# Performance work log

Hardware: AMD Instinct MI355X
Metric: run time of the kernel (lower is better)

The kernel has to match this reference:

```python
import jax, jax.numpy as jnp
import numpy as np

N = 100000   # nodes
E = 1600000  # edges (before self-loops)
D = 128      # in_feats
H = 128      # n_hidden


def setup_inputs() -> dict:
    key = jax.random.key(0)
    k = jax.random.split(key, 6)
    x = jax.random.normal(k[0], (N, D), dtype=jnp.float32)
    src = jax.random.randint(k[1], (E,), 0, N, dtype=jnp.int32)
    dst = jax.random.randint(k[2], (E,), 0, N, dtype=jnp.int32)
    W1 = jax.random.normal(k[3], (D, H), dtype=jnp.float32) / np.float32(np.sqrt(D))
    b1 = jnp.zeros((H,), jnp.float32)
    W2 = jax.random.normal(k[4], (H, H), dtype=jnp.float32) / np.float32(np.sqrt(H))
    b2 = jnp.zeros((H,), jnp.float32)
    return {"x": x, "src": src, "dst": dst, "W1": W1, "b1": b1, "W2": W2, "b2": b2}


def _gcn(x, src, dst, W1, b1, W2, b2):
    n = x.shape[0]
    # add_self_loop(g)
    loops = jnp.arange(n, dtype=src.dtype)
    s = jnp.concatenate([src, loops])
    d = jnp.concatenate([dst, loops])
    ones = jnp.ones((s.shape[0],), dtype=x.dtype)
    deg_out = jax.ops.segment_sum(ones, s, num_segments=n)  # src out-degree
    deg_in = jax.ops.segment_sum(ones, d, num_segments=n)   # dst in-degree
    # DGL GraphConv norm='both': D_out^{-1/2} on source side, D_in^{-1/2} on dest side
    norm_out = jax.lax.rsqrt(jnp.maximum(deg_out, 1.0))[:, None]
    norm_in = jax.lax.rsqrt(jnp.maximum(deg_in, 1.0))[:, None]

    def layer(h, W, b):
        h = h * norm_out                                   # [n, f]
        agg = jax.ops.segment_sum(h[s], d, num_segments=n)  # gather + scatter-add over edges
        return (agg * norm_in) @ W + b

    h = layer(x, W1, b1)
    # dropout p=0 -> identity
    h = layer(h, W2, b2)
    return h


def reference(x, src, dst, W1, b1, W2, b2):
    return _gcn(x, src, dst, W1, b1, W2, b2)
```

## Files before the change

kernel.cpp:

```cpp
#include <hip/hip_runtime.h>

#define FD 128
#define SHIFT 10
#define BNODES 1024
#define NBK 128
#define CHUNK 4096
#define ST 512
#define NE 12

typedef unsigned int u32;
typedef unsigned short u16;
typedef unsigned char u8;
typedef __attribute__((ext_vector_type(8))) short short8;
typedef __attribute__((ext_vector_type(4))) float f32x4;
typedef __attribute__((ext_vector_type(4))) u32 u32x4;

__device__ inline u16 f2bf(float f) {
  u32 u = __float_as_uint(f);
  u += 0x7fffu + ((u >> 16) & 1u);
  return (u16)(u >> 16);
}
__device__ inline float bf2f(u16 h) { return __uint_as_float((u32)h << 16); }

__global__ __launch_bounds__(512) void k_hist(const int* __restrict__ src,
                                              const int* __restrict__ dst,
                                              int* __restrict__ bcntD,
                                              int* __restrict__ bcntS,
                                              int e, int n, int nbuck) {
  __shared__ int shD[NBK];
  __shared__ int shS[NBK];
  int tid = threadIdx.x;
  if (tid < NBK) { shD[tid] = 0; shS[tid] = 0; }
  __syncthreads();
  int total = e + n;
  for (int t = blockIdx.x * blockDim.x + tid; t < total; t += gridDim.x * blockDim.x) {
    if (t < e) {
      atomicAdd(&shD[dst[t] >> SHIFT], 1);
      atomicAdd(&shS[src[t] >> SHIFT], 1);
    } else {
      atomicAdd(&shD[(t - e) >> SHIFT], 1);
    }
  }
  __syncthreads();
  if (tid < nbuck) {
    if (shD[tid]) atomicAdd(&bcntD[tid], shD[tid]);
    if (shS[tid]) atomicAdd(&bcntS[tid], shS[tid]);
  }
}

__global__ __launch_bounds__(NBK) void k_bscan(
    const int* __restrict__ bcntD, const int* __restrict__ bcntS,
    int* __restrict__ bbaseD, int* __restrict__ bcurD,
    int* __restrict__ bbaseS, int* __restrict__ bcurS,
    int nbuck, int totalD, int totalS) {
  __shared__ int shD[NBK];
  __shared__ int shS[NBK];
  int tid = threadIdx.x;
  int vD = (tid < nbuck) ? bcntD[tid] : 0;
  int vS = (tid < nbuck) ? bcntS[tid] : 0;
  shD[tid] = vD; shS[tid] = vS;
  __syncthreads();
  for (int off = 1; off < NBK; off <<= 1) {
    int aD = (tid >= off) ? shD[tid - off] : 0;
    int aS = (tid >= off) ? shS[tid - off] : 0;
    __syncthreads();
    shD[tid] += aD; shS[tid] += aS;
    __syncthreads();
  }
  if (tid < nbuck) {
    int exD = shD[tid] - vD; bbaseD[tid] = exD; bcurD[tid] = exD;
    int exS = shS[tid] - vS; bbaseS[tid] = exS; bcurS[tid] = exS;
  }
  if (tid == 0) { bbaseD[nbuck] = totalD; bbaseS[nbuck] = totalS; }
}

__global__ __launch_bounds__(ST) void k_scatter(
    const int* __restrict__ src, const int* __restrict__ dst,
    int* __restrict__ bcurD, int* __restrict__ bcurS,
    u32* __restrict__ pairs, u16* __restrict__ pairs2,
    int e, int n, int nbuck) {
  __shared__ int histD[NBK], exclD[NBK], gbaseD[NBK], rankD[NBK];
  __shared__ int histS[NBK], exclS[NBK], gbaseS[NBK], rankS[NBK];
  __shared__ u32 stgv[CHUNK];
  __shared__ u8  stgb[CHUNK];
  __shared__ u16 stg2[CHUNK];
  __shared__ u8  stg2b[CHUNK];
  int tid = threadIdx.x;
  int c0 = blockIdx.x * CHUNK;
  int total = e + n;
  if (tid < NBK) { histD[tid] = 0; histS[tid] = 0; }
  __syncthreads();
  u32 pv_[8]; int bD_[8], bS_[8]; bool v_[8], vs_[8];
  #pragma unroll
  for (int i = 0; i < 8; ++i) {
    int t = c0 + i * ST + tid;
    v_[i] = (t < total);
    vs_[i] = (t < e);
    pv_[i] = 0; bD_[i] = 0; bS_[i] = 0;
    if (v_[i]) {
      int s, d;
      if (vs_[i]) { s = src[t]; d = dst[t]; }
      else        { s = t - e;  d = s; }
      pv_[i] = ((u32)(d & (BNODES - 1)) << 22) | (u32)s;
      bD_[i] = d >> SHIFT;
      atomicAdd(&histD[bD_[i]], 1);
      if (vs_[i]) { bS_[i] = s >> SHIFT; atomicAdd(&histS[bS_[i]], 1); }
    }
  }
  __syncthreads();
  int hD = 0, hS = 0;
  if (tid < NBK) { hD = histD[tid]; hS = histS[tid]; }
  __syncthreads();
  for (int off = 1; off < NBK; off <<= 1) {
    int aD = 0, aS = 0;
    if (tid < NBK && tid >= off) { aD = histD[tid - off]; aS = histS[tid - off]; }
    __syncthreads();
    if (tid < NBK) { histD[tid] += aD; histS[tid] += aS; }
    __syncthreads();
  }
  if (tid < NBK) {
    int exD = histD[tid] - hD; exclD[tid] = exD; rankD[tid] = exD;
    int exS = histS[tid] - hS; exclS[tid] = exS; rankS[tid] = exS;
    gbaseD[tid] = (tid < nbuck && hD > 0) ? atomicAdd(&bcurD[tid], hD) : 0;
    gbaseS[tid] = (tid < nbuck && hS > 0) ? atomicAdd(&bcurS[tid], hS) : 0;
  }
  __syncthreads();
  #pragma unroll
  for (int i = 0; i < 8; ++i) {
    if (v_[i]) {
      int p = atomicAdd(&rankD[bD_[i]], 1);
      stgv[p] = pv_[i];
      stgb[p] = (u8)bD_[i];
    }
    if (vs_[i]) {
      int p = atomicAdd(&rankS[bS_[i]], 1);
      stg2[p] = (u16)(pv_[i] & (BNODES - 1));
      stg2b[p] = (u8)bS_[i];
    }
  }
  __syncthreads();
  int V = min(CHUNK, total - c0);
  for (int j = tid; j < V; j += ST) {
    int b = stgb[j];
    pairs[gbaseD[b] + (j - exclD[b])] = stgv[j];
  }
  int V2 = min(CHUNK, e - c0);
  for (int j = tid; j < V2; j += ST) {
    int b = stg2b[j];
    pairs2[gbaseS[b] + (j - exclS[b])] = stg2[j];
  }
}

__global__ __launch_bounds__(1024) void k_build(
    const u32* __restrict__ pairs, const int* __restrict__ bbase,
    const u16* __restrict__ pairs2, const int* __restrict__ bbaseS,
    int* __restrict__ rp, int* __restrict__ col,
    float* __restrict__ nin, float* __restrict__ nout,
    int n, int nbuck, int total) {
  __shared__ int cnt[BNODES];
  __shared__ int off_[BNODES];
  __shared__ int cur[BNODES];
  int tid = threadIdx.x;
  if (blockIdx.x >= (unsigned)nbuck) {
    int b = blockIdx.x - nbuck;
    int base = bbaseS[b], end = bbaseS[b + 1];
    cnt[tid] = 0;
    __syncthreads();
    for (int t = base + tid; t < end; t += 1024)
      atomicAdd(&cnt[(int)pairs2[t]], 1);
    __syncthreads();
    int node = (b << SHIFT) + tid;
    if (node < n) nout[node] = rsqrtf((float)(cnt[tid] + 1));
    return;
  }
  int b = blockIdx.x;
  int base = bbase[b], end = bbase[b + 1];
  int node0 = b << SHIFT;
  cnt[tid] = 0;
  __syncthreads();
  for (int t = base + tid; t < end; t += 1024)
    atomicAdd(&cnt[(int)(pairs[t] >> 22)], 1);
  __syncthreads();
  int c = cnt[tid];
  off_[tid] = c;
  __syncthreads();
  for (int off = 1; off < BNODES; off <<= 1) {
    int add = (tid >= off) ? off_[tid - off] : 0;
    __syncthreads();
    off_[tid] += add;
    __syncthreads();
  }
  int ex = off_[tid] - c;
  int node = node0 + tid;
  if (node < n) {
    rp[node] = base + ex;
    nin[node] = rsqrtf((float)c);
  }
  if (b == nbuck - 1 && tid == 0) rp[n] = total;
  cur[tid] = ex;
  __syncthreads();
  for (int t = base + tid; t < end; t += 1024) {
    u32 pr = pairs[t];
    int p = atomicAdd(&cur[(int)(pr >> 22)], 1);
    col[base + p] = (int)(pr & 0x3FFFFFu);
  }
}

__global__ __launch_bounds__(256) void k_prescale(
    const float* __restrict__ x, const float* __restrict__ nout,
    u32* __restrict__ xs, int n) {
  int tot = (n + 1) * 64;
  const float2* xv = (const float2*)x;
  for (int idx = blockIdx.x * blockDim.x + threadIdx.x; idx < tot;
       idx += gridDim.x * blockDim.x) {
    int row = idx >> 6;
    if (row >= n) { xs[idx] = 0; }
    else {
      float w = nout[row];
      float2 v = xv[idx];
      xs[idx] = (u32)f2bf(v.x * w) | ((u32)f2bf(v.y * w) << 16);
    }
  }
}

__global__ void k_prepw(const float* __restrict__ W1, u32* __restrict__ wf1hi,
                        u32* __restrict__ wf1lo,
                        const float* __restrict__ W2, u32* __restrict__ wf2hi,
                        u32* __restrict__ wf2lo) {
  int gi = blockIdx.x * 256 + threadIdx.x;
  int i = gi & 8191;
  const float* W = (gi < 8192) ? W1 : W2;
  u32* wfhi = (gi < 8192) ? wf1hi : wf2hi;
  u32* wflo = (gi < 8192) ? wf1lo : wf2lo;
  int m = i & 3, l = (i >> 2) & 63, f = i >> 8;
  int kt = f & 3, nt = f >> 2;
  int k0 = kt * 32 + ((l >> 4) << 3) + 2 * m;
  int c = nt * 16 + (l & 15);
  float w0 = W[k0 * FD + c], w1 = W[(k0 + 1) * FD + c];
  u16 h0 = f2bf(w0), h1 = f2bf(w1);
  u16 l0 = f2bf(w0 - bf2f(h0)), l1 = f2bf(w1 - bf2f(h1));
  wfhi[i] = (u32)h0 | ((u32)h1 << 16);
  wflo[i] = (u32)l0 | ((u32)l1 << 16);
}

__global__ __launch_bounds__(256) void k_layer(
    const u32* __restrict__ hs, const int* __restrict__ rp,
    const int* __restrict__ col, const float* __restrict__ nin,
    const u32* __restrict__ wfhi, const u32* __restrict__ wflo,
    const float* __restrict__ bias, const float* __restrict__ nout,
    float* __restrict__ fout, u32* __restrict__ hsout, int n, int mode) {
  __shared__ u32 As[1024];
  int tid = threadIdx.x;
  int lane = tid & 63;
  int wv = tid >> 6;
  int g = lane >> 4, ch = lane & 15;
  int r0 = blockIdx.x * 16;
  int lr = wv * 4 + g;
  int r = r0 + lr;
  bool valid = (r < n);

  int e0 = 0, e1 = 0;
  if (valid) { e0 = rp[r]; e1 = rp[r + 1]; }
  int m = e1 - e0;
  m = max(m, __shfl_xor(m, 16, 64));
  m = max(m, __shfl_xor(m, 32, 64));
  int trips = (m + NE - 1) / NE;
  float acc[8] = {0.f, 0.f, 0.f, 0.f, 0.f, 0.f, 0.f, 0.f};
  const u32x4* hv = (const u32x4*)hs;
  int em1 = (e1 > 0) ? (e1 - 1) : 0;

  int cs[NE], csn[NE];
  #pragma unroll
  for (int u = 0; u < NE; ++u) cs[u] = col[min(e0 + u, em1)];
  for (int it = 0; it < trips; ++it) {
    int tb = e0 + it * NE;
    u32x4 buf[NE];
    #pragma unroll
    for (int u = 0; u < NE; ++u) {
      int s = (tb + u < e1) ? cs[u] : n;
      buf[u] = hv[(size_t)s * 16 + ch];
    }
    #pragma unroll
    for (int u = 0; u < NE; ++u) csn[u] = col[min(tb + NE + u, em1)];
    __builtin_amdgcn_sched_barrier(0);
    #pragma unroll
    for (int u = 0; u < NE; ++u)
      #pragma unroll
      for (int j = 0; j < 4; ++j) {
        u32 x = buf[u][j];
        acc[2 * j]     += __uint_as_float(x << 16);
        acc[2 * j + 1] += __uint_as_float(x & 0xFFFF0000u);
      }
    #pragma unroll
    for (int u = 0; u < NE; ++u) cs[u] = csn[u];
  }
  float wi = valid ? nin[r] : 0.f;
  u32 hi[4];
  #pragma unroll
  for (int j = 0; j < 4; ++j) {
    float v0 = acc[2 * j] * wi, v1 = acc[2 * j + 1] * wi;
    hi[j] = (u32)f2bf(v0) | ((u32)f2bf(v1) << 16);
  }
  int sch = ch ^ (lr & 7);
  u32x4 hq = {hi[0], hi[1], hi[2], hi[3]};
  *(u32x4*)(As + lr * 64 + sch * 4) = hq;
  __syncthreads();

  short8 afh[4];
  int arow = lane & 15;
  #pragma unroll
  for (int kt = 0; kt < 4; ++kt) {
    int boff = arow * 256 + ((kt * 64 + (lane >> 4) * 16) ^ ((arow & 7) << 4));
    afh[kt] = *(const short8*)((const char*)As + boff);
  }
  __syncthreads();

  #pragma unroll
  for (int q = 0; q < 2; ++q) {
    int nt = wv * 2 + q;
    f32x4 oacc = {0.f, 0.f, 0.f, 0.f};
    #pragma unroll
    for (int kt = 0; kt < 4; ++kt) {
      int f = nt * 4 + kt;
      short8 wh = *(const short8*)(wfhi + (size_t)(f * 64 + lane) * 4);
      short8 wl = *(const short8*)(wflo + (size_t)(f * 64 + lane) * 4);
      oacc = __builtin_amdgcn_mfma_f32_16x16x32_bf16(afh[kt], wh, oacc, 0, 0, 0);
      oacc = __builtin_amdgcn_mfma_f32_16x16x32_bf16(afh[kt], wl, oacc, 0, 0, 0);
    }
    int c = nt * 16 + (lane & 15);
    float bv = bias[c];
    int rbase = r0 + (lane >> 4) * 4;
    if (mode == 0) {
      #pragma unroll
      for (int j = 0; j < 4; ++j) {
        int row = rbase + j;
        if (row < n) fout[(size_t)row * FD + c] = oacc[j] + bv;
      }
    } else {
      #pragma unroll
      for (int j = 0; j < 4; ++j) {
        int row = rbase + j;
        float w = (row < n) ? nout[row] : 0.f;
        ((u16*)As)[(row - r0) * 128 + c] = f2bf((oacc[j] + bv) * w);
      }
    }
  }
  if (mode == 1) {
    __syncthreads();
    int row = tid >> 4, chk = tid & 15;
    if (r0 + row < n)
      *(u32x4*)(hsout + (size_t)(r0 + row) * 64 + chk * 4) =
          *(const u32x4*)(As + row * 64 + chk * 4);
  }
}

extern "C" void kernel_launch(void* const* d_in, const int* in_sizes, int n_in,
                              void* d_out, int out_size, void* d_ws, size_t ws_size,
                              hipStream_t stream) {
  const float* x  = (const float*)d_in[0];
  const int* src  = (const int*)d_in[1];
  const int* dst  = (const int*)d_in[2];
  const float* W1 = (const float*)d_in[3];
  const float* b1 = (const float*)d_in[4];
  const float* W2 = (const float*)d_in[5];
  const float* b2 = (const float*)d_in[6];
  float* out = (float*)d_out;

  int n = in_sizes[0] / FD;
  int e = in_sizes[1];
  int total = e + n;
  int nbuck = (n + BNODES - 1) >> SHIFT;

  char* ws = (char*)d_ws;
  size_t off = 0;
  auto alloc = [&](size_t bytes) -> void* {
    void* p = ws + off;
    off += (bytes + 255) / 256 * 256;
    return p;
  };
  u32* xs    = (u32*)alloc((size_t)(n + 16) * 64 * 4);
  u32* pairs = xs;
  u32* h1s   = (u32*)alloc((size_t)(n + 16) * 64 * 4);
  u16* pairs2 = (u16*)alloc((size_t)e * 2 + 256);
  int* col   = (int*)alloc((size_t)total * 4 + 256);
  int* rp    = (int*)alloc((size_t)(n + 1) * 4);
  float* nin  = (float*)alloc((size_t)n * 4);
  float* nout = (float*)alloc((size_t)n * 4);
  int* bcntD  = (int*)alloc(NBK * 4);
  int* bcntS  = (int*)alloc(NBK * 4);
  int* bbaseD = (int*)alloc((NBK + 1) * 4);
  int* bbaseS = (int*)alloc((NBK + 1) * 4);
  int* bcurD  = (int*)alloc(NBK * 4);
  int* bcurS  = (int*)alloc(NBK * 4);
  u32* wf1hi  = (u32*)alloc(8192 * 4);
  u32* wf1lo  = (u32*)alloc(8192 * 4);
  u32* wf2hi  = (u32*)alloc(8192 * 4);
  u32* wf2lo  = (u32*)alloc(8192 * 4);

  hipMemsetAsync(bcntD, 0, (size_t)NBK * 4 * 2, stream);
  hipMemsetAsync(h1s + (size_t)n * 64, 0, FD * 2, stream);

  k_hist<<<256, 512, 0, stream>>>(src, dst, bcntD, bcntS, e, n, nbuck);
  k_bscan<<<1, NBK, 0, stream>>>(bcntD, bcntS, bbaseD, bcurD, bbaseS, bcurS,
                                 nbuck, total, e);
  k_scatter<<<(total + CHUNK - 1) / CHUNK, ST, 0, stream>>>(
      src, dst, bcurD, bcurS, pairs, pairs2, e, n, nbuck);
  k_build<<<2 * nbuck, 1024, 0, stream>>>(pairs, bbaseD, pairs2, bbaseS,
                                          rp, col, nin, nout, n, nbuck, total);
  k_prepw<<<64, 256, 0, stream>>>(W1, wf1hi, wf1lo, W2, wf2hi, wf2lo);
  k_prescale<<<2048, 256, 0, stream>>>(x, nout, xs, n);

  int lgrid = (n + 15) / 16;
  k_layer<<<lgrid, 256, 0, stream>>>(xs, rp, col, nin, wf1hi, wf1lo, b1, nout,
                                     nullptr, h1s, n, 1);
  k_layer<<<lgrid, 256, 0, stream>>>(h1s, rp, col, nin, wf2hi, wf2lo,
                                     b2, nout, out, nullptr, n, 0);
}
```

Baseline: 228.5 us.

## Sort nodes by in-degree so each wave processes rows of similar length

Adds a degree histogram in k_build, a scan kernel and a permutation kernel that orders nodes by capped in-degree. The layer kernels then process rows through this permutation, so each wave's max-degree loop trip count matches its rows' actual work and divergence is reduced. The edge unroll depth drops from 12 to 8 to suit the shorter, more uniform loops. In exchange it adds two small kernels, an extra indirection per row, and scattered output writes, which lose the locality of writing consecutive rows.

```diff
diff --git a/kernel.cpp b/kernel.cpp
--- a/kernel.cpp
+++ b/kernel.cpp
@@ -6,7 +6,8 @@
 #define NBK 128
 #define CHUNK 4096
 #define ST 512
-#define NE 12
+#define NE 8
+#define DMAX 256
 
 typedef unsigned int u32;
 typedef unsigned short u16;
@@ -156,10 +157,12 @@
     const u16* __restrict__ pairs2, const int* __restrict__ bbaseS,
     int* __restrict__ rp, int* __restrict__ col,
     float* __restrict__ nin, float* __restrict__ nout,
+    u16* __restrict__ deg16, int* __restrict__ dhist,
     int n, int nbuck, int total) {
   __shared__ int cnt[BNODES];
   __shared__ int off_[BNODES];
   __shared__ int cur[BNODES];
+  __shared__ int ddh[DMAX];
   int tid = threadIdx.x;
   if (blockIdx.x >= (unsigned)nbuck) {
     int b = blockIdx.x - nbuck;
@@ -177,6 +180,7 @@
   int base = bbase[b], end = bbase[b + 1];
   int node0 = b << SHIFT;
   cnt[tid] = 0;
+  if (tid < DMAX) ddh[tid] = 0;
   __syncthreads();
   for (int t = base + tid; t < end; t += 1024)
     atomicAdd(&cnt[(int)(pairs[t] >> 22)], 1);
@@ -195,14 +199,53 @@
   if (node < n) {
     rp[node] = base + ex;
     nin[node] = rsqrtf((float)c);
+    int dc = min(c, DMAX - 1);
+    deg16[node] = (u16)dc;
+    atomicAdd(&ddh[dc], 1);
   }
   if (b == nbuck - 1 && tid == 0) rp[n] = total;
   cur[tid] = ex;
   __syncthreads();
+  if (tid < DMAX && ddh[tid]) atomicAdd(&dhist[tid], ddh[tid]);
   for (int t = base + tid; t < end; t += 1024) {
     u32 pr = pairs[t];
     int p = atomicAdd(&cur[(int)(pr >> 22)], 1);
     col[base + p] = (int)(pr & 0x3FFFFFu);
+  }
+}
+
+__global__ __launch_bounds__(DMAX) void k_dscan(const int* __restrict__ dhist,
+                                                int* __restrict__ dcur) {
+  __shared__ int sh[DMAX];
+  int tid = threadIdx.x;
+  int v = dhist[tid];
+  sh[tid] = v;
+  __syncthreads();
+  for (int off = 1; off < DMAX; off <<= 1) {
+    int a = (tid >= off) ? sh[tid - off] : 0;
+    __syncthreads();
+    sh[tid] += a;
+    __syncthreads();
+  }
+  dcur[tid] = sh[tid] - v;
+}
+
+__global__ __launch_bounds__(1024) void k_perm(const u16* __restrict__ deg16,
+                                               int* __restrict__ dcur,
+                                               int* __restrict__ perm, int n) {
+  __shared__ int lh[DMAX], lb[DMAX], lr2[DMAX];
+  int tid = threadIdx.x;
+  int node = blockIdx.x * 1024 + tid;
+  int d = (node < n) ? (int)deg16[node] : -1;
+  if (tid < DMAX) { lh[tid] = 0; lr2[tid] = 0; }
+  __syncthreads();
+  if (d >= 0) atomicAdd(&lh[d], 1);
+  __syncthreads();
+  if (tid < DMAX && lh[tid]) lb[tid] = atomicAdd(&dcur[tid], lh[tid]);
+  __syncthreads();
+  if (d >= 0) {
+    int rk = atomicAdd(&lr2[d], 1);
+    perm[lb[d] + rk] = node;
   }
 }
 
@@ -246,6 +289,7 @@
 __global__ __launch_bounds__(256) void k_layer(
     const u32* __restrict__ hs, const int* __restrict__ rp,
     const int* __restrict__ col, const float* __restrict__ nin,
+    const int* __restrict__ perm,
     const u32* __restrict__ wfhi, const u32* __restrict__ wflo,
     const float* __restrict__ bias, const float* __restrict__ nout,
     float* __restrict__ fout, u32* __restrict__ hsout, int n, int mode) {
@@ -256,11 +300,12 @@
   int g = lane >> 4, ch = lane & 15;
   int r0 = blockIdx.x * 16;
   int lr = wv * 4 + g;
-  int r = r0 + lr;
-  bool valid = (r < n);
+  int rl = r0 + lr;
+  bool valid = (rl < n);
+  int row = valid ? perm[rl] : n;
 
   int e0 = 0, e1 = 0;
-  if (valid) { e0 = rp[r]; e1 = rp[r + 1]; }
+  if (valid) { e0 = rp[row]; e1 = rp[row + 1]; }
   int m = e1 - e0;
   m = max(m, __shfl_xor(m, 16, 64));
   m = max(m, __shfl_xor(m, 32, 64));
@@ -294,7 +339,7 @@
     #pragma unroll
     for (int u = 0; u < NE; ++u) cs[u] = csn[u];
   }
-  float wi = valid ? nin[r] : 0.f;
+  float wi = valid ? nin[row] : 0.f;
   u32 hi[4];
   #pragma unroll
   for (int j = 0; j < 4; ++j) {
@@ -333,24 +378,25 @@
     if (mode == 0) {
       #pragma unroll
       for (int j = 0; j < 4; ++j) {
-        int row = rbase + j;
-        if (row < n) fout[(size_t)row * FD + c] = oacc[j] + bv;
+        int rl2 = rbase + j;
+        if (rl2 < n) fout[(size_t)perm[rl2] * FD + c] = oacc[j] + bv;
       }
     } else {
       #pragma unroll
       for (int j = 0; j < 4; ++j) {
-        int row = rbase + j;
-        float w = (row < n) ? nout[row] : 0.f;
-        ((u16*)As)[(row - r0) * 128 + c] = f2bf((oacc[j] + bv) * w);
+        int rl2 = rbase + j;
+        float w = (rl2 < n) ? nout[perm[rl2]] : 0.f;
+        ((u16*)As)[(rl2 - r0) * 128 + c] = f2bf((oacc[j] + bv) * w);
       }
     }
   }
   if (mode == 1) {
     __syncthreads();
-    int row = tid >> 4, chk = tid & 15;
-    if (r0 + row < n)
-      *(u32x4*)(hsout + (size_t)(r0 + row) * 64 + chk * 4) =
-          *(const u32x4*)(As + row * 64 + chk * 4);
+    int lrow = tid >> 4, chk = tid & 15;
+    int rl2 = r0 + lrow;
+    if (rl2 < n)
+      *(u32x4*)(hsout + (size_t)perm[rl2] * 64 + chk * 4) =
+          *(const u32x4*)(As + lrow * 64 + chk * 4);
   }
 }
 
@@ -386,8 +432,12 @@
   int* rp    = (int*)alloc((size_t)(n + 1) * 4);
   float* nin  = (float*)alloc((size_t)n * 4);
   float* nout = (float*)alloc((size_t)n * 4);
+  u16* deg16  = (u16*)alloc((size_t)n * 2);
+  int* perm   = (int*)alloc((size_t)n * 4);
   int* bcntD  = (int*)alloc(NBK * 4);
   int* bcntS  = (int*)alloc(NBK * 4);
+  int* dhist  = (int*)alloc(DMAX * 4);
+  int* dcur   = (int*)alloc(DMAX * 4);
   int* bbaseD = (int*)alloc((NBK + 1) * 4);
   int* bbaseS = (int*)alloc((NBK + 1) * 4);
   int* bcurD  = (int*)alloc(NBK * 4);
@@ -397,7 +447,7 @@
   u32* wf2hi  = (u32*)alloc(8192 * 4);
   u32* wf2lo  = (u32*)alloc(8192 * 4);
 
-  hipMemsetAsync(bcntD, 0, (size_t)NBK * 4 * 2, stream);
+  hipMemsetAsync(bcntD, 0, (size_t)(NBK * 2 + DMAX) * 4, stream);
   hipMemsetAsync(h1s + (size_t)n * 64, 0, FD * 2, stream);
 
   k_hist<<<256, 512, 0, stream>>>(src, dst, bcntD, bcntS, e, n, nbuck);
@@ -406,13 +456,16 @@
   k_scatter<<<(total + CHUNK - 1) / CHUNK, ST, 0, stream>>>(
       src, dst, bcurD, bcurS, pairs, pairs2, e, n, nbuck);
   k_build<<<2 * nbuck, 1024, 0, stream>>>(pairs, bbaseD, pairs2, bbaseS,
-                                          rp, col, nin, nout, n, nbuck, total);
+                                          rp, col, nin, nout, deg16, dhist,
+                                          n, nbuck, total);
+  k_dscan<<<1, DMAX, 0, stream>>>(dhist, dcur);
+  k_perm<<<nbuck, 1024, 0, stream>>>(deg16, dcur, perm, n);
   k_prepw<<<64, 256, 0, stream>>>(W1, wf1hi, wf1lo, W2, wf2hi, wf2lo);
   k_prescale<<<2048, 256, 0, stream>>>(x, nout, xs, n);
 
   int lgrid = (n + 15) / 16;
-  k_layer<<<lgrid, 256, 0, stream>>>(xs, rp, col, nin, wf1hi, wf1lo, b1, nout,
-                                     nullptr, h1s, n, 1);
-  k_layer<<<lgrid, 256, 0, stream>>>(h1s, rp, col, nin, wf2hi, wf2lo,
+  k_layer<<<lgrid, 256, 0, stream>>>(xs, rp, col, nin, perm, wf1hi, wf1lo, b1,
+                                     nout, nullptr, h1s, n, 1);
+  k_layer<<<lgrid, 256, 0, stream>>>(h1s, rp, col, nin, perm, wf2hi, wf2lo,
                                      b2, nout, out, nullptr, n, 0);
 }
```

Result: slower. 248.4 us (+8.7%).

## Make each wave own 16 rows end-to-end, removing block-level barriers in GCN layer

Applied to the files above, without the earlier changes.

The layer kernel now gives each wavefront its own 16-row tile. The wave aggregates its rows in four sequential passes of 4 rows, then runs all 8 MFMA column tiles itself from a private LDS slice, using only lgkmcnt waits instead of __syncthreads. Each block covers 64 rows with 4x the LDS, and the gather unroll drops from 12 to 8. This removes block-wide barriers and the cross-wave dependency. In exchange, each wave does the full weight-fragment loads (8 column tiles instead of 2), and the gather runs serially over four row groups with less memory-level parallelism per trip.

```diff
diff --git a/kernel.cpp b/kernel.cpp
--- a/kernel.cpp
+++ b/kernel.cpp
@@ -6,7 +6,7 @@
 #define NBK 128
 #define CHUNK 4096
 #define ST 512
-#define NE 12
+#define NE 8
 
 typedef unsigned int u32;
 typedef unsigned short u16;
@@ -249,75 +249,86 @@
     const u32* __restrict__ wfhi, const u32* __restrict__ wflo,
     const float* __restrict__ bias, const float* __restrict__ nout,
     float* __restrict__ fout, u32* __restrict__ hsout, int n, int mode) {
-  __shared__ u32 As[1024];
+  __shared__ u32 As[4096];
   int tid = threadIdx.x;
   int lane = tid & 63;
   int wv = tid >> 6;
   int g = lane >> 4, ch = lane & 15;
-  int r0 = blockIdx.x * 16;
-  int lr = wv * 4 + g;
-  int r = r0 + lr;
-  bool valid = (r < n);
-
-  int e0 = 0, e1 = 0;
-  if (valid) { e0 = rp[r]; e1 = rp[r + 1]; }
-  int m = e1 - e0;
-  m = max(m, __shfl_xor(m, 16, 64));
-  m = max(m, __shfl_xor(m, 32, 64));
-  int trips = (m + NE - 1) / NE;
-  float acc[8] = {0.f, 0.f, 0.f, 0.f, 0.f, 0.f, 0.f, 0.f};
+  int wbase = (blockIdx.x * 4 + wv) * 16;
+  u32* Aw = As + wv * 1024;
   const u32x4* hv = (const u32x4*)hs;
-  int em1 = (e1 > 0) ? (e1 - 1) : 0;
-
-  int cs[NE], csn[NE];
-  #pragma unroll
-  for (int u = 0; u < NE; ++u) cs[u] = col[min(e0 + u, em1)];
-  for (int it = 0; it < trips; ++it) {
-    int tb = e0 + it * NE;
-    u32x4 buf[NE];
+
+  #pragma unroll 1
+  for (int b = 0; b < 4; ++b) {
+    int lr = b * 4 + g;
+    int r = wbase + lr;
+    bool valid = (r < n);
+    int e0 = 0, e1 = 0;
+    if (valid) { e0 = rp[r]; e1 = rp[r + 1]; }
+    int m = e1 - e0;
+    m = max(m, __shfl_xor(m, 16, 64));
+    m = max(m, __shfl_xor(m, 32, 64));
+    int trips = (m + NE - 1) / NE;
+    float acc[8] = {0.f, 0.f, 0.f, 0.f, 0.f, 0.f, 0.f, 0.f};
+    int em1 = (e1 > 0) ? (e1 - 1) : 0;
+    int cs[NE], csn[NE];
     #pragma unroll
-    for (int u = 0; u < NE; ++u) {
-      int s = (tb + u < e1) ? cs[u] : n;
-      buf[u] = hv[(size_t)s * 16 + ch];
-    }
+    for (int u = 0; u < NE; ++u) cs[u] = col[min(e0 + u, em1)];
+    for (int it = 0; it < trips; ++it) {
+      int tb = e0 + it * NE;
+      u32x4 buf[NE];
+      #pragma unroll
+      for (int u = 0; u < NE; ++u) {
+        int s = (tb + u < e1) ? cs[u] : n;
+        buf[u] = hv[(size_t)s * 16 + ch];
+      }
+      #pragma unroll
+      for (int u = 0; u < NE; ++u) csn[u] = col[min(tb + NE + u, em1)];
+      __builtin_amdgcn_sched_barrier(0);
+      #pragma unroll
+      for (int u = 0; u < NE; ++u)
+        #pragma unroll
+        for (int j = 0; j < 4; ++j) {
+          u32 x = buf[u][j];
+          acc[2 * j]     += __uint_as_float(x << 16);
+          acc[2 * j + 1] += __uint_as_float(x & 0xFFFF0000u);
+        }
+      #pragma unroll
+      for (int u = 0; u < NE; ++u) cs[u] = csn[u];
+    }
+    float wi = valid ? nin[r] : 0.f;
+    u32 hi[4];
     #pragma unroll
-    for (int u = 0; u < NE; ++u) csn[u] = col[min(tb + NE + u, em1)];
-    __builtin_amdgcn_sched_barrier(0);
-    #pragma unroll
-    for (int u = 0; u < NE; ++u)
-      #pragma unroll
-      for (int j = 0; j < 4; ++j) {
-        u32 x = buf[u][j];
-        acc[2 * j]     += __uint_as_float(x << 16);
-        acc[2 * j + 1] += __uint_as_float(x & 0xFFFF0000u);
-      }
-    #pragma unroll
-    for (int u = 0; u < NE; ++u) cs[u] = csn[u];
-  }
-  float wi = valid ? nin[r] : 0.f;
-  u32 hi[4];
-  #pragma unroll
-  for (int j = 0; j < 4; ++j) {
-    float v0 = acc[2 * j] * wi, v1 = acc[2 * j + 1] * wi;
-    hi[j] = (u32)f2bf(v0) | ((u32)f2bf(v1) << 16);
-  }
-  int sch = ch ^ (lr & 7);
-  u32x4 hq = {hi[0], hi[1], hi[2], hi[3]};
-  *(u32x4*)(As + lr * 64 + sch * 4) = hq;
-  __syncthreads();
+    for (int j = 0; j < 4; ++j) {
+      float v0 = acc[2 * j] * wi, v1 = acc[2 * j + 1] * wi;
+      hi[j] = (u32)f2bf(v0) | ((u32)f2bf(v1) << 16);
+    }
+    int sch = ch ^ (lr & 7);
+    u32x4 hq = {hi[0], hi[1], hi[2], hi[3]};
+    *(u32x4*)(Aw + lr * 64 + sch * 4) = hq;
+  }
+
+  asm volatile("s_waitcnt lgkmcnt(0)" ::: "memory");
+  __builtin_amdgcn_sched_barrier(0);
 
   short8 afh[4];
   int arow = lane & 15;
   #pragma unroll
   for (int kt = 0; kt < 4; ++kt) {
     int boff = arow * 256 + ((kt * 64 + (lane >> 4) * 16) ^ ((arow & 7) << 4));
-    afh[kt] = *(const short8*)((const char*)As + boff);
-  }
-  __syncthreads();
-
-  #pragma unroll
-  for (int q = 0; q < 2; ++q) {
-    int nt = wv * 2 + q;
+    afh[kt] = *(const short8*)((const char*)Aw + boff);
+  }
+
+  float wout[4];
+  int rb0 = wbase + (lane >> 4) * 4;
+  if (mode == 1) {
+    #pragma unroll
+    for (int j = 0; j < 4; ++j)
+      wout[j] = (rb0 + j < n) ? nout[rb0 + j] : 0.f;
+  }
+
+  #pragma unroll 1
+  for (int nt = 0; nt < 8; ++nt) {
     f32x4 oacc = {0.f, 0.f, 0.f, 0.f};
     #pragma unroll
     for (int kt = 0; kt < 4; ++kt) {
@@ -329,28 +340,32 @@
     }
     int c = nt * 16 + (lane & 15);
     float bv = bias[c];
-    int rbase = r0 + (lane >> 4) * 4;
     if (mode == 0) {
       #pragma unroll
       for (int j = 0; j < 4; ++j) {
-        int row = rbase + j;
+        int row = rb0 + j;
         if (row < n) fout[(size_t)row * FD + c] = oacc[j] + bv;
       }
     } else {
       #pragma unroll
       for (int j = 0; j < 4; ++j) {
-        int row = rbase + j;
-        float w = (row < n) ? nout[row] : 0.f;
-        ((u16*)As)[(row - r0) * 128 + c] = f2bf((oacc[j] + bv) * w);
+        int lr2 = (lane >> 4) * 4 + j;
+        ((u16*)Aw)[lr2 * 128 + c] = f2bf((oacc[j] + bv) * wout[j]);
       }
     }
   }
   if (mode == 1) {
-    __syncthreads();
-    int row = tid >> 4, chk = tid & 15;
-    if (r0 + row < n)
-      *(u32x4*)(hsout + (size_t)(r0 + row) * 64 + chk * 4) =
-          *(const u32x4*)(As + row * 64 + chk * 4);
+    asm volatile("s_waitcnt lgkmcnt(0)" ::: "memory");
+    __builtin_amdgcn_sched_barrier(0);
+    #pragma unroll
+    for (int it = 0; it < 4; ++it) {
+      int ci = it * 64 + lane;
+      int lrow = ci >> 4, chk = ci & 15;
+      int row = wbase + lrow;
+      if (row < n)
+        *(u32x4*)(hsout + (size_t)row * 64 + chk * 4) =
+            *(const u32x4*)(Aw + lrow * 64 + chk * 4);
+    }
   }
 }
 
@@ -410,7 +425,7 @@
   k_prepw<<<64, 256, 0, stream>>>(W1, wf1hi, wf1lo, W2, wf2hi, wf2lo);
   k_prescale<<<2048, 256, 0, stream>>>(x, nout, xs, n);
 
-  int lgrid = (n + 15) / 16;
+  int lgrid = (n + 63) / 64;
   k_layer<<<lgrid, 256, 0, stream>>>(xs, rp, col, nin, wf1hi, wf1lo, b1, nout,
                                      nullptr, h1s, n, 1);
   k_layer<<<lgrid, 256, 0, stream>>>(h1s, rp, col, nin, wf2hi, wf2lo,
```

Result: slower. 235.4 us (+3.0%).
